# Performance work log

Hardware: AMD Instinct MI355X
Metric: run time of the kernel (lower is better)

## Reference

```python
import jax, jax.numpy as jnp
import numpy as np

B = 32768
D_VIS, D_LANG, D_STATE = 256, 128, 128
D_MODEL, N_EXP, TOP_K = 512, 8, 2
D_IN = D_VIS + D_LANG + D_STATE
EPS = 1e-5

def _gelu(x):
    # torch nn.GELU default = exact erf form
    return jax.nn.gelu(x, approximate=False)

def _ln(x, g, b):
    mu = x.mean(-1, keepdims=True)
    var = ((x - mu) ** 2).mean(-1, keepdims=True)
    return (x - mu) / jnp.sqrt(var + EPS) * g + b

def setup_inputs() -> dict:
    key = jax.random.key(0)
    ks = jax.random.split(key, 16)
    f32 = jnp.float32
    def w(k, shape, fan_in):
        return jax.random.normal(k, shape, dtype=f32) * (1.0 / np.sqrt(fan_in))
    return {
        "vis":   jax.random.normal(ks[0], (B, D_VIS), dtype=f32),
        "lang":  jax.random.normal(ks[1], (B, D_LANG), dtype=f32),
        "state": jax.random.normal(ks[2], (B, D_STATE), dtype=f32),
        # fusion: Linear(D_IN, D_MODEL) + LayerNorm + GELU
        "Wf": w(ks[3], (D_IN, D_MODEL), D_IN),
        "bf": jnp.zeros((D_MODEL,), f32),
        "gf": jnp.ones((D_MODEL,), f32),
        "betaf": jnp.zeros((D_MODEL,), f32),
        # gate (bias-free); random instead of torch's zeros-init so routing is non-degenerate
        "Wg": w(ks[4], (D_MODEL, N_EXP), D_MODEL),
        # stacked expert params: d -> 2d -> d -> d, residual LayerNorm
        "W1": w(ks[5], (N_EXP, D_MODEL, 2 * D_MODEL), D_MODEL),
        "b1": jnp.zeros((N_EXP, 2 * D_MODEL), f32),
        "W2": w(ks[6], (N_EXP, 2 * D_MODEL, D_MODEL), 2 * D_MODEL),
        "b2": jnp.zeros((N_EXP, D_MODEL), f32),
        "W3": w(ks[7], (N_EXP, D_MODEL, D_MODEL), D_MODEL),
        "b3": jnp.zeros((N_EXP, D_MODEL), f32),
        "ge": jnp.ones((N_EXP, D_MODEL), f32),
        "be": jnp.zeros((N_EXP, D_MODEL), f32),
    }

def reference(vis, lang, state, Wf, bf, gf, betaf, Wg, W1, b1, W2, b2, W3, b3, ge, be):
    # fusion projection  [B, D_IN] -> [B, D_MODEL]
    x = _gelu(_ln(jnp.concatenate([vis, lang, state], axis=-1) @ Wf + bf, gf, betaf))
    logits = x @ Wg                              # [B, E]
    all_probs = jax.nn.softmax(logits, axis=-1)  # [B, E]
    top_vals, top_idx = jax.lax.top_k(logits, TOP_K)   # [B, K]
    top_w = jax.nn.softmax(top_vals, axis=-1)          # [B, K]
    # per-(token, expert) combine weight: sum_k top_w[b,k] * [top_idx[b,k]==e]
    onehot = jax.nn.one_hot(top_idx, N_EXP, dtype=x.dtype)   # [B, K, E]
    combine = (onehot * top_w[..., None]).sum(axis=1)        # [B, E]
    out = jnp.zeros_like(x)
    for e in range(N_EXP):  # small fixed expert count; dense compute, sparse combine
        h = _gelu(x @ W1[e] + b1[e])
        h = _gelu(h @ W2[e] + b2[e])
        h = h @ W3[e] + b3[e]
        y = _ln(x + h, ge[e], be[e])            # Expert: ln(x + net(x))
        out = out + combine[:, e:e + 1] * y
    # load-balancing aux loss (counts carry no gradient, as in torch scatter_add of ones)
    counts = onehot.sum(axis=(0, 1))            # [E]
    f_i = counts / (B * TOP_K)
    lb_loss = N_EXP * jnp.sum(f_i * all_probs.mean(axis=0))
    return out, lb_loss
```

## Files before the change

kernel.cpp:

```cpp
#include <hip/hip_runtime.h>
#include <math.h>

typedef __bf16     bf16x8 __attribute__((ext_vector_type(8)));
typedef _Float16   f16x8  __attribute__((ext_vector_type(8)));
typedef float      f32x4  __attribute__((ext_vector_type(4)));
typedef unsigned short u16x8 __attribute__((ext_vector_type(8)));

#define DEVI __device__ __forceinline__
constexpr int B_TOK = 32768;
constexpr int MAXT  = 520;
constexpr int NBLK  = B_TOK / 16;

DEVI unsigned short f2bf(float f){
  unsigned int u = __builtin_bit_cast(unsigned int, f);
  u += 0x7fffu + ((u >> 16) & 1u);
  return (unsigned short)(u >> 16);
}
DEVI float bf2f(unsigned short b){
  return __builtin_bit_cast(float, (unsigned int)b << 16);
}
DEVI float gelu_fast(float x){
  float z = fabsf(x) * 0.70710678118654752f;
  float t = __builtin_amdgcn_rcpf(1.f + 0.3275911f * z);
  float p = t*(0.254829592f + t*(-0.284496736f + t*(1.421413741f + t*(-1.453152027f + t*1.061405429f))));
  float e = __expf(-z * z);
  float erfz = 1.f - p * e;
  float s = copysignf(erfz, x);
  return 0.5f * x * (1.f + s);
}
DEVI void load16_lds(const void* g, void* l){
  __builtin_amdgcn_global_load_lds(
      (const __attribute__((address_space(1))) unsigned int*)g,
      (__attribute__((address_space(3))) unsigned int*)l, 16, 0, 0);
}
DEVI float wredsum(float v){
#pragma unroll
  for (int off = 32; off > 0; off >>= 1) v += __shfl_xor(v, off, 64);
  return v;
}

__global__ void transpose_cast_bf16_k(const float* __restrict__ src, unsigned short* __restrict__ dst,
                                      int R, int C){
  __shared__ float tile[32][33];
  size_t base = (size_t)blockIdx.z * R * C;
  int c0 = blockIdx.x * 32, r0 = blockIdx.y * 32;
  for (int i = threadIdx.y; i < 32; i += 8)
    tile[i][threadIdx.x] = src[base + (size_t)(r0 + i) * C + c0 + threadIdx.x];
  __syncthreads();
  for (int i = threadIdx.y; i < 32; i += 8)
    dst[base + (size_t)(c0 + i) * R + r0 + threadIdx.x] = f2bf(tile[threadIdx.x][i]);
}

__global__ void transpose_split_f16_k(const float* __restrict__ src, unsigned short* __restrict__ dh,
                                      unsigned short* __restrict__ dl, int R, int C){
  __shared__ float tile[32][33];
  int c0 = blockIdx.x * 32, r0 = blockIdx.y * 32;
  for (int i = threadIdx.y; i < 32; i += 8)
    tile[i][threadIdx.x] = src[(size_t)(r0 + i) * C + c0 + threadIdx.x];
  __syncthreads();
  for (int i = threadIdx.y; i < 32; i += 8){
    float f = tile[threadIdx.x][i];
    _Float16 h = (_Float16)f;
    _Float16 l = (_Float16)(f - (float)h);
    size_t o = (size_t)(c0 + i) * R + r0 + threadIdx.x;
    dh[o] = __builtin_bit_cast(unsigned short, h);
    dl[o] = __builtin_bit_cast(unsigned short, l);
  }
}

__global__ __launch_bounds__(256, 2) void gemm_fusion_f16split(
    const float* __restrict__ vis, const float* __restrict__ lang, const float* __restrict__ state,
    const unsigned short* __restrict__ Wh, const unsigned short* __restrict__ Wl,
    const float* __restrict__ bias, float* __restrict__ Xpre)
{
  constexpr int K = 512, N = 512;
  __shared__ alignas(16) unsigned short smemF[32768];
  unsigned short* AhS = smemF;
  unsigned short* AlS = smemF + 8192;
  unsigned short* BhS = smemF + 16384;
  unsigned short* BlS = smemF + 24576;
  const int tid = threadIdx.x;
  const int row_s = tid >> 3, col_s = (tid & 7) * 8;
  const int swz = (row_s & 7) << 3;
  const unsigned short *pbh[4], *pbl[4];
  int arow[4];
#pragma unroll
  for (int i = 0; i < 4; ++i){
    arow[i] = blockIdx.x * 128 + i * 32 + row_s;
    size_t br = (size_t)(blockIdx.y * 128 + i * 32 + row_s) * K + (col_s ^ swz);
    pbh[i] = Wh + br; pbl[i] = Wl + br;
  }
  const int w = tid >> 6, lane = tid & 63;
  const int wr = (w >> 1) * 64, wc = (w & 1) * 64;
  const int lm = lane & 15, lk8 = (lane >> 4) * 8;
  const int fxor = (lm & 7) << 3;
  f32x4 acc[4][4] = {};
  for (int k0 = 0; k0 < K; k0 += 64){
#pragma unroll
    for (int i = 0; i < 4; ++i){
      load16_lds(pbh[i] + k0, &BhS[i*2048 + tid*8]);
      load16_lds(pbl[i] + k0, &BlS[i*2048 + tid*8]);
    }
    int col = k0 + col_s;
#pragma unroll
    for (int i = 0; i < 4; ++i){
      const float* src;
      if (col < 256)      src = vis   + (size_t)arow[i] * 256 + col;
      else if (col < 384) src = lang  + (size_t)arow[i] * 128 + (col - 256);
      else                src = state + (size_t)arow[i] * 128 + (col - 384);
      float4 a = *(const float4*)src, b = *(const float4*)(src + 4);
      float f[8] = {a.x, a.y, a.z, a.w, b.x, b.y, b.z, b.w};
      u16x8 hh, ll;
#pragma unroll
      for (int j = 0; j < 8; ++j){
        _Float16 h = (_Float16)f[j];
        _Float16 l = (_Float16)(f[j] - (float)h);
        hh[j] = __builtin_bit_cast(unsigned short, h);
        ll[j] = __builtin_bit_cast(unsigned short, l);
      }
      *(u16x8*)&AhS[i*2048 + row_s*64 + (col_s ^ swz)] = hh;
      *(u16x8*)&AlS[i*2048 + row_s*64 + (col_s ^ swz)] = ll;
    }
    __syncthreads();
#pragma unroll
    for (int kk = 0; kk < 64; kk += 32){
      f16x8 fah[4], fal[4], fbh[4], fbl[4];
#pragma unroll
      for (int m = 0; m < 4; ++m){
        int ro = (wr + m*16 + lm) * 64 + ((kk + lk8) ^ fxor);
        fah[m] = *(const f16x8*)&AhS[ro];
        fal[m] = *(const f16x8*)&AlS[ro];
      }
#pragma unroll
      for (int n = 0; n < 4; ++n){
        int ro = (wc + n*16 + lm) * 64 + ((kk + lk8) ^ fxor);
        fbh[n] = *(const f16x8*)&BhS[ro];
        fbl[n] = *(const f16x8*)&BlS[ro];
      }
#pragma unroll
      for (int m = 0; m < 4; ++m)
#pragma unroll
        for (int n = 0; n < 4; ++n){
          acc[m][n] = __builtin_amdgcn_mfma_f32_16x16x32_f16(fah[m], fbh[n], acc[m][n], 0, 0, 0);
          acc[m][n] = __builtin_amdgcn_mfma_f32_16x16x32_f16(fal[m], fbh[n], acc[m][n], 0, 0, 0);
          acc[m][n] = __builtin_amdgcn_mfma_f32_16x16x32_f16(fah[m], fbl[n], acc[m][n], 0, 0, 0);
        }
    }
    __syncthreads();
  }
  float* Cs = (float*)smemF;
  const int lk4 = (lane >> 4) * 4;
#pragma unroll
  for (int n = 0; n < 4; ++n){
    float bv = bias[blockIdx.y * 128 + wc + n*16 + lm];
#pragma unroll
    for (int m = 0; m < 4; ++m)
#pragma unroll
      for (int r = 0; r < 4; ++r){
        int rr = wr + m*16 + lk4 + r;
        Cs[rr * 128 + ((wc + n*16 + lm) ^ ((rr & 7) << 2))] = acc[m][n][r] + bv;
      }
  }
  __syncthreads();
#pragma unroll
  for (int j = 0; j < 16; ++j){
    int r = j*8 + (tid >> 5), c = (tid & 31) * 4;
    float4 v = *(const float4*)&Cs[r*128 + (c ^ ((r & 7) << 2))];
    *(float4*)&Xpre[(size_t)(blockIdx.x*128 + r) * N + blockIdx.y*128 + c] = v;
  }
}

template<int K, int N, int NT, bool GATHER, bool GELU_ACT, bool GLOBAL_ROW>
__global__ __launch_bounds__(256, 2) void egemm_k(
    const unsigned short* __restrict__ A, const int* __restrict__ rowlist,
    const int* __restrict__ cnt, const int* __restrict__ nTilesP,
    const int* __restrict__ tileE, const int* __restrict__ tileR0,
    int chunkBase, int chunkTiles, int tpg,
    const unsigned short* __restrict__ W, const float* __restrict__ bias,
    unsigned short* __restrict__ Cout)
{
  const int g = blockIdx.x & 7;
  const int j = blockIdx.x >> 3;
  const int tloc = g * tpg + j / NT;
  const int ntile = j % NT;
  if (tloc >= chunkTiles) return;
  const int t = chunkBase + tloc;
  if (t >= nTilesP[0]) return;
  const int e = tileE[t], r0 = tileR0[t];
  int rows = cnt[e] - r0; rows = rows > 128 ? 128 : rows;
  __shared__ alignas(16) unsigned short smem[16384];
  unsigned short* As = smem;
  unsigned short* Bs = smem + 8192;
  const int tid = threadIdx.x;
  const int row_s = tid >> 3, col_s = (tid & 7) * 8;
  const int swz = (row_s & 7) << 3;
  const unsigned short *pa[4], *pb[4];
#pragma unroll
  for (int i = 0; i < 4; ++i){
    int ir = i * 32 + row_s;
    size_t arow;
    if (GATHER){
      int rr = ir < rows ? ir : rows - 1;
      arow = (size_t)rowlist[(size_t)e * B_TOK + r0 + rr];
    } else {
      arow = (size_t)tloc * 128 + ir;
    }
    pa[i] = A + arow * K + (col_s ^ swz);
    pb[i] = W + (size_t)e * ((size_t)N * K) + (size_t)(ntile * 128 + ir) * K + (col_s ^ swz);
  }
  const int w = tid >> 6, lane = tid & 63;
  const int wr = (w >> 1) * 64, wc = (w & 1) * 64;
  const int lm = lane & 15, lk8 = (lane >> 4) * 8;
  const int fxor = (lm & 7) << 3;
  f32x4 acc[4][4] = {};
  for (int k0 = 0; k0 < K; k0 += 64){
#pragma unroll
    for (int i = 0; i < 4; ++i) load16_lds(pa[i] + k0, &As[i*2048 + tid*8]);
#pragma unroll
    for (int i = 0; i < 4; ++i) load16_lds(pb[i] + k0, &Bs[i*2048 + tid*8]);
    __syncthreads();
#pragma unroll
    for (int kk = 0; kk < 64; kk += 32){
      bf16x8 a[4], b[4];
#pragma unroll
      for (int m = 0; m < 4; ++m)
        a[m] = *(const bf16x8*)&As[(wr + m*16 + lm)*64 + ((kk + lk8) ^ fxor)];
#pragma unroll
      for (int n = 0; n < 4; ++n)
        b[n] = *(const bf16x8*)&Bs[(wc + n*16 + lm)*64 + ((kk + lk8) ^ fxor)];
#pragma unroll
      for (int m = 0; m < 4; ++m)
#pragma unroll
        for (int n = 0; n < 4; ++n)
          acc[m][n] = __builtin_amdgcn_mfma_f32_16x16x32_bf16(a[m], b[n], acc[m][n], 0, 0, 0);
    }
    __syncthreads();
  }
  unsigned short* Cs = smem;
  const int lk4 = (lane >> 4) * 4;
#pragma unroll
  for (int n = 0; n < 4; ++n){
    float bv = bias[(size_t)e * N + ntile * 128 + wc + n*16 + lm];
#pragma unroll
    for (int m = 0; m < 4; ++m)
#pragma unroll
      for (int r = 0; r < 4; ++r){
        float v = acc[m][n][r] + bv;
        if (GELU_ACT) v = gelu_fast(v);
        int rr = wr + m*16 + lk4 + r;
        Cs[rr * 128 + ((wc + n*16 + lm) ^ ((rr & 7) << 3))] = f2bf(v);
      }
  }
  __syncthreads();
  const size_t outTile = GLOBAL_ROW ? (size_t)t * 128 : (size_t)tloc * 128;
#pragma unroll
  for (int jj = 0; jj < 8; ++jj){
    int r = jj*16 + (tid >> 4), c = (tid & 15) * 8;
    if (r < rows){
      u16x8 v = *(const u16x8*)&Cs[r*128 + (c ^ ((r & 7) << 3))];
      *(u16x8*)&Cout[(outTile + r) * N + ntile*128 + c] = v;
    }
  }
}

__global__ __launch_bounds__(256) void ln_gelu_gate_k(
    const float* __restrict__ Xpre, const float* __restrict__ gf,
    const float* __restrict__ betaf, const float* __restrict__ Wg,
    unsigned short* __restrict__ Xbf, int* __restrict__ PK,
    int* __restrict__ BlockCnt, float* __restrict__ BlockProbs)
{
  __shared__ float s_probs[8];
  __shared__ int s_cnt[8];
  __shared__ int s_pk[16];
  __shared__ float s_w[16];
  const int tid = threadIdx.x, wv = tid >> 6, lane = tid & 63;
  if (tid < 8){ s_probs[tid] = 0.f; s_cnt[tid] = 0; }
  __syncthreads();
  float gg[8], bb[8], wg[8][8];
  {
    const float4* gp = (const float4*)(gf + lane * 8);
    const float4* bp = (const float4*)(betaf + lane * 8);
    float4 g0 = gp[0], g1 = gp[1], c0 = bp[0], c1 = bp[1];
    gg[0]=g0.x; gg[1]=g0.y; gg[2]=g0.z; gg[3]=g0.w; gg[4]=g1.x; gg[5]=g1.y; gg[6]=g1.z; gg[7]=g1.w;
    bb[0]=c0.x; bb[1]=c0.y; bb[2]=c0.z; bb[3]=c0.w; bb[4]=c1.x; bb[5]=c1.y; bb[6]=c1.z; bb[7]=c1.w;
#pragma unroll
    for (int j = 0; j < 8; ++j){
      const float4* wrow = (const float4*)(Wg + (size_t)(lane * 8 + j) * 8);
      float4 w0 = wrow[0], w1 = wrow[1];
      wg[j][0]=w0.x; wg[j][1]=w0.y; wg[j][2]=w0.z; wg[j][3]=w0.w;
      wg[j][4]=w1.x; wg[j][5]=w1.y; wg[j][6]=w1.z; wg[j][7]=w1.w;
    }
  }
  float4 vv[4][2];
#pragma unroll
  for (int it = 0; it < 4; ++it){
    const int row = blockIdx.x * 16 + wv * 4 + it;
    const float* xp = Xpre + (size_t)row * 512 + lane * 8;
    vv[it][0] = *(const float4*)xp;
    vv[it][1] = *(const float4*)(xp + 4);
  }
#pragma unroll
  for (int it = 0; it < 4; ++it){
    const int tloc = wv * 4 + it;
    const int row = blockIdx.x * 16 + tloc;
    float v[8] = {vv[it][0].x, vv[it][0].y, vv[it][0].z, vv[it][0].w,
                  vv[it][1].x, vv[it][1].y, vv[it][1].z, vv[it][1].w};
    float s1 = 0.f, s2 = 0.f;
#pragma unroll
    for (int j = 0; j < 8; ++j){ s1 += v[j]; s2 += v[j]*v[j]; }
    {
      float sel = (lane & 1) ? s1 : s2;
      float r = __shfl_xor(sel, 1, 64);
      float tt = ((lane & 1) ? s2 : s1) + r;
#pragma unroll
      for (int off = 2; off < 64; off <<= 1) tt += __shfl_xor(tt, off, 64);
      float other = __shfl_xor(tt, 1, 64);
      s1 = (lane & 1) ? other : tt;
      s2 = (lane & 1) ? tt : other;
    }
    const float mu  = s1 * (1.f / 512.f);
    const float var = s2 * (1.f / 512.f) - mu * mu;
    const float inv = 1.f / sqrtf(var + 1e-5f);
    float o[8];
#pragma unroll
    for (int j = 0; j < 8; ++j)
      o[j] = gelu_fast((v[j] - mu) * inv * gg[j] + bb[j]);
    u16x8 ob;
#pragma unroll
    for (int j = 0; j < 8; ++j) ob[j] = f2bf(o[j]);
    *(u16x8*)(Xbf + (size_t)row * 512 + lane * 8) = ob;
    float acc[8] = {0.f,0.f,0.f,0.f,0.f,0.f,0.f,0.f};
#pragma unroll
    for (int j = 0; j < 8; ++j)
#pragma unroll
      for (int e = 0; e < 8; ++e) acc[e] += o[j] * wg[j][e];
    float v4[4], v2[2], v1f;
#pragma unroll
    for (int i = 0; i < 4; ++i){
      float sel = (lane & 1) ? acc[i] : acc[i+4];
      float r = __shfl_xor(sel, 1, 64);
      v4[i] = ((lane & 1) ? acc[i+4] : acc[i]) + r;
    }
#pragma unroll
    for (int i = 0; i < 2; ++i){
      float sel = (lane & 2) ? v4[i] : v4[i+2];
      float r = __shfl_xor(sel, 2, 64);
      v2[i] = ((lane & 2) ? v4[i+2] : v4[i]) + r;
    }
    {
      float sel = (lane & 4) ? v2[0] : v2[1];
      float r = __shfl_xor(sel, 4, 64);
      v1f = ((lane & 4) ? v2[1] : v2[0]) + r;
    }
#pragma unroll
    for (int off = 8; off < 64; off <<= 1) v1f += __shfl_xor(v1f, off, 64);
    float lg[8];
#pragma unroll
    for (int e = 0; e < 8; ++e){
      int src = (lane & 56) | ((e >> 2) & 1) | (((e >> 1) & 1) << 1) | ((e & 1) << 2);
      lg[e] = __shfl(v1f, src, 64);
    }
    float mx = lg[0];
#pragma unroll
    for (int e = 1; e < 8; ++e) mx = fmaxf(mx, lg[e]);
    float pe[8], ps = 0.f;
#pragma unroll
    for (int e = 0; e < 8; ++e){ pe[e] = __expf(lg[e] - mx); ps += pe[e]; }
    float invp = 1.f / ps;
    int i1 = 0;
#pragma unroll
    for (int e = 1; e < 8; ++e) if (lg[e] > lg[i1]) i1 = e;
    int i2 = (i1 == 0) ? 1 : 0;
#pragma unroll
    for (int e = 0; e < 8; ++e) if (e != i1 && lg[e] > lg[i2]) i2 = e;
    float wA = 1.f / (1.f + __expf(lg[i2] - lg[i1]));
    if (lane == 0){
#pragma unroll
      for (int e = 0; e < 8; ++e) atomicAdd(&s_probs[e], pe[e] * invp);
      int r0 = atomicAdd(&s_cnt[i1], 1);
      int r1 = atomicAdd(&s_cnt[i2], 1);
      s_pk[tloc] = i1 | (r0 << 3) | (i2 << 8) | (r1 << 16);
      s_w[tloc] = wA;
    }
  }
  __syncthreads();
  if (tid < 8){
    BlockCnt[blockIdx.x * 8 + tid] = s_cnt[tid];
    BlockProbs[blockIdx.x * 8 + tid] = s_probs[tid];
  }
  if (tid < 16){
    int t = blockIdx.x * 16 + tid;
    PK[2*t]   = s_pk[tid];
    PK[2*t+1] = __builtin_bit_cast(int, s_w[tid]);
  }
}

__global__ __launch_bounds__(256) void scan_k(
    const int* __restrict__ BlockCnt, const float* __restrict__ BlockProbs,
    int* __restrict__ BlockBase, int* __restrict__ CNT, int* __restrict__ nTiles,
    int* __restrict__ tileE, int* __restrict__ tileR0, int* __restrict__ rowBase,
    float* __restrict__ lbOut)
{
  __shared__ int sS[8][256];
  __shared__ float sF[8][256];
  __shared__ int sTot[8];
  __shared__ float sProbTot[8];
  __shared__ int sTileBase[9];
  const int tid = threadIdx.x;
  int local[8][8];
  int sum[8] = {0,0,0,0,0,0,0,0};
  float fsum[8] = {0.f,0.f,0.f,0.f,0.f,0.f,0.f,0.f};
#pragma unroll
  for (int jb = 0; jb < 8; ++jb){
    int blk = tid * 8 + jb;
#pragma unroll
    for (int e = 0; e < 8; ++e){
      int c = BlockCnt[blk*8 + e];
      local[jb][e] = c;
      sum[e] += c;
      fsum[e] += BlockProbs[blk*8 + e];
    }
  }
#pragma unroll
  for (int e = 0; e < 8; ++e){ sS[e][tid] = sum[e]; sF[e][tid] = fsum[e]; }
  __syncthreads();
  for (int off = 1; off < 256; off <<= 1){
    int add[8];
#pragma unroll
    for (int e = 0; e < 8; ++e) add[e] = (tid >= off) ? sS[e][tid - off] : 0;
    __syncthreads();
#pragma unroll
    for (int e = 0; e < 8; ++e) sS[e][tid] += add[e];
    __syncthreads();
  }
  for (int off = 128; off > 0; off >>= 1){
    if (tid < off)
#pragma unroll
      for (int e = 0; e < 8; ++e) sF[e][tid] += sF[e][tid + off];
    __syncthreads();
  }
  int base[8];
#pragma unroll
  for (int e = 0; e < 8; ++e) base[e] = (tid == 0) ? 0 : sS[e][tid-1];
#pragma unroll
  for (int jb = 0; jb < 8; ++jb){
    int blk = tid * 8 + jb;
#pragma unroll
    for (int e = 0; e < 8; ++e){ BlockBase[blk*8 + e] = base[e]; base[e] += local[jb][e]; }
  }
  if (tid == 0){
    int t = 0;
    float acc = 0.f;
    for (int e = 0; e < 8; ++e){
      int c = sS[e][255]; c = c < 0 ? 0 : (c > B_TOK ? B_TOK : c);
      sTot[e] = c;
      CNT[e] = c;
      sTileBase[e] = t;
      rowBase[e] = t * 128;
      t += (c + 127) >> 7;
      acc += ((float)c / (float)(B_TOK * 2)) * (sF[e][0] / (float)B_TOK);
    }
    sTileBase[8] = t;
    nTiles[0] = t;
    lbOut[0] = 8.f * acc;
  }
  __syncthreads();
  const int ntot = sTileBase[8];
  for (int i = tid; i < MAXT; i += 256){
    int e = 0;
#pragma unroll
    for (int k = 1; k <= 8; ++k) if (i >= sTileBase[k]) e = k;
    if (i < ntot){ tileE[i] = e; tileR0[i] = (i - sTileBase[e]) * 128; }
    else { tileE[i] = 0; tileR0[i] = 0; }
  }
}

__global__ __launch_bounds__(256) void place_k(
    const int* __restrict__ PK, const int* __restrict__ BlockBase,
    int* __restrict__ rowlist, int* __restrict__ TS, float* __restrict__ TW)
{
  const int t = blockIdx.x * 256 + threadIdx.x;
  int pk = PK[2*t];
  float w0 = __builtin_bit_cast(float, PK[2*t+1]);
  int e0 = pk & 7, r0 = (pk >> 3) & 31;
  int e1 = (pk >> 8) & 7, r1 = (pk >> 16) & 31;
  int blk = t >> 4;
  int p0 = BlockBase[blk*8 + e0] + r0;
  int p1 = BlockBase[blk*8 + e1] + r1;
  rowlist[(size_t)e0 * B_TOK + p0] = t;
  rowlist[(size_t)e1 * B_TOK + p1] = t;
  TS[2*t]   = (e0 << 15) | p0;  TW[2*t]   = w0;
  TS[2*t+1] = (e1 << 15) | p1;  TW[2*t+1] = 1.f - w0;
}

__global__ __launch_bounds__(256) void combine_k(
    const unsigned short* __restrict__ Xbf, const unsigned short* __restrict__ H3F,
    const int* __restrict__ TS, const float* __restrict__ TW,
    const int* __restrict__ rowBase, const float* __restrict__ ge,
    const float* __restrict__ be, float* __restrict__ out)
{
  const int tok = blockIdx.x * 4 + (threadIdx.x >> 6);
  const int lane = threadIdx.x & 63;
  u16x8 xb = *(const u16x8*)(Xbf + (size_t)tok * 512 + lane * 8);
  float x[8];
#pragma unroll
  for (int j = 0; j < 8; ++j) x[j] = bf2f(xb[j]);
  float o[8] = {0.f,0.f,0.f,0.f,0.f,0.f,0.f,0.f};
#pragma unroll
  for (int kslot = 0; kslot < 2; ++kslot){
    int sl = TS[tok*2 + kslot];
    float wgt = TW[tok*2 + kslot];
    int e = sl >> 15, p = sl & 32767;
    size_t hrow = (size_t)(rowBase[e] + p);
    u16x8 hb = *(const u16x8*)(H3F + hrow * 512 + lane * 8);
    float s[8];
#pragma unroll
    for (int j = 0; j < 8; ++j) s[j] = x[j] + bf2f(hb[j]);
    float sm = 0.f;
#pragma unroll
    for (int j = 0; j < 8; ++j) sm += s[j];
    sm = wredsum(sm);
    float mu = sm * (1.f / 512.f);
    float q = 0.f;
#pragma unroll
    for (int j = 0; j < 8; ++j){ float d = s[j] - mu; q += d * d; }
    q = wredsum(q);
    float inv = 1.f / sqrtf(q * (1.f / 512.f) + 1e-5f);
    const float4* gp = (const float4*)(ge + (size_t)e * 512 + lane * 8);
    const float4* bp = (const float4*)(be + (size_t)e * 512 + lane * 8);
    float4 g0 = gp[0], g1 = gp[1], c0 = bp[0], c1 = bp[1];
    float gg[8] = {g0.x,g0.y,g0.z,g0.w,g1.x,g1.y,g1.z,g1.w};
    float bb[8] = {c0.x,c0.y,c0.z,c0.w,c1.x,c1.y,c1.z,c1.w};
#pragma unroll
    for (int j = 0; j < 8; ++j)
      o[j] += wgt * ((s[j]-mu)*inv*gg[j] + bb[j]);
  }
  float* op = out + (size_t)tok * 512 + lane * 8;
  *(float4*)op       = make_float4(o[0], o[1], o[2], o[3]);
  *(float4*)(op + 4) = make_float4(o[4], o[5], o[6], o[7]);
}

extern "C" void kernel_launch(void* const* d_in, const int* in_sizes, int n_in,
                              void* d_out, int out_size, void* d_ws, size_t ws_size,
                              hipStream_t stream)
{
  (void)in_sizes; (void)n_in; (void)out_size;
  const float* vis   = (const float*)d_in[0];
  const float* lang  = (const float*)d_in[1];
  const float* state = (const float*)d_in[2];
  const float* Wf    = (const float*)d_in[3];
  const float* bf    = (const float*)d_in[4];
  const float* gf    = (const float*)d_in[5];
  const float* betaf = (const float*)d_in[6];
  const float* Wg    = (const float*)d_in[7];
  const float* W1    = (const float*)d_in[8];
  const float* b1    = (const float*)d_in[9];
  const float* W2    = (const float*)d_in[10];
  const float* b2    = (const float*)d_in[11];
  const float* W3    = (const float*)d_in[12];
  const float* b3    = (const float*)d_in[13];
  const float* ge    = (const float*)d_in[14];
  const float* be    = (const float*)d_in[15];

  char* ws = (char*)d_ws;
  size_t off = 0;
  auto alloc = [&](size_t n){ size_t o = off; off += (n + 255) & ~(size_t)255; return o; };

  unsigned short* WFH  = (unsigned short*)(ws + alloc((size_t)512*512*2));
  unsigned short* WFL  = (unsigned short*)(ws + alloc((size_t)512*512*2));
  unsigned short* W1T  = (unsigned short*)(ws + alloc((size_t)8*1024*512*2));
  unsigned short* W2T  = (unsigned short*)(ws + alloc((size_t)8*512*1024*2));
  unsigned short* W3T  = (unsigned short*)(ws + alloc((size_t)8*512*512*2));
  unsigned short* XBF  = (unsigned short*)(ws + alloc((size_t)B_TOK*512*2));
  int*            RLIST= (int*)(ws + alloc((size_t)8*B_TOK*4));
  int*            TS   = (int*)(ws + alloc((size_t)B_TOK*2*4));
  float*          TW   = (float*)(ws + alloc((size_t)B_TOK*2*4));
  int*            PK   = (int*)(ws + alloc((size_t)B_TOK*2*4));
  int*            BCNT = (int*)(ws + alloc((size_t)NBLK*8*4));
  float*          BPROB= (float*)(ws + alloc((size_t)NBLK*8*4));
  int*            BBASE= (int*)(ws + alloc((size_t)NBLK*8*4));
  int*            CNT  = (int*)(ws + alloc(64));
  int*            NT_  = (int*)(ws + alloc(64));
  int*            RB   = (int*)(ws + alloc(64));
  int*            TE   = (int*)(ws + alloc(MAXT*4));
  int*            TR   = (int*)(ws + alloc(MAXT*4));
  unsigned short* H3F  = (unsigned short*)(ws + alloc((size_t)MAXT*128*512*2));

  const size_t perTile = (size_t)128*1024*2 + (size_t)128*512*2;
  size_t remain = (ws_size > off) ? (ws_size - off) : 0;
  int tch, nch;
  size_t need2 = (size_t)260 * perTile, need4 = (size_t)B_TOK*512*4;
  if (remain >= need2 && need2 >= need4){ tch = 260; nch = 2; }
  else { tch = 130; nch = 4; }
  size_t regB = alloc(need2 > need4 ? (nch == 2 ? need2 : need4) : need4);
  float*          XPRE = (float*)(ws + regB);
  unsigned short* H1   = (unsigned short*)(ws + regB);
  unsigned short* H2   = H1 + (size_t)tch*128*1024;
  const int tpg = (tch + 7) / 8;

  transpose_split_f16_k<<<dim3(16,16,1), dim3(32,8), 0, stream>>>(Wf, WFH, WFL, 512, 512);
  transpose_cast_bf16_k<<<dim3(32,16,8), dim3(32,8), 0, stream>>>(W1, W1T, 512, 1024);
  transpose_cast_bf16_k<<<dim3(16,32,8), dim3(32,8), 0, stream>>>(W2, W2T, 1024, 512);
  transpose_cast_bf16_k<<<dim3(16,16,8), dim3(32,8), 0, stream>>>(W3, W3T, 512, 512);
  gemm_fusion_f16split<<<dim3(256,4), 256, 0, stream>>>(vis, lang, state, WFH, WFL, bf, XPRE);
  ln_gelu_gate_k<<<NBLK, 256, 0, stream>>>(XPRE, gf, betaf, Wg, XBF, PK, BCNT, BPROB);
  scan_k<<<1, 256, 0, stream>>>(BCNT, BPROB, BBASE, CNT, NT_, TE, TR, RB,
                                ((float*)d_out) + (size_t)B_TOK*512);
  place_k<<<B_TOK/256, 256, 0, stream>>>(PK, BBASE, RLIST, TS, TW);

  for (int c = 0; c < nch; ++c){
    int cb = c * tch;
    egemm_k<512, 1024, 8, true,  true,  false><<<dim3(8*tpg*8), 256, 0, stream>>>(
        XBF, RLIST, CNT, NT_, TE, TR, cb, tch, tpg, W1T, b1, H1);
    egemm_k<1024, 512, 4, false, true,  false><<<dim3(8*tpg*4), 256, 0, stream>>>(
        H1,  RLIST, CNT, NT_, TE, TR, cb, tch, tpg, W2T, b2, H2);
    egemm_k<512,  512, 4, false, false, true ><<<dim3(8*tpg*4), 256, 0, stream>>>(
        H2,  RLIST, CNT, NT_, TE, TR, cb, tch, tpg, W3T, b3, H3F);
  }
  combine_k<<<B_TOK/4, 256, 0, stream>>>(XBF, H3F, TS, TW, RB, ge, be, (float*)d_out);
}
```

Baseline: 470.5 us.

## Fuse fusion GEMM with LayerNorm, GELU and gating into one kernel

The fusion projection GEMM now computes full 512-wide rows per 128-token block with 512 threads. LayerNorm, GELU, gate logits, softmax and top-2 selection run in the epilogue from registers. This removes the fp32 Xpre round trip through global memory and a separate kernel launch. Routing blocks grow from 16 to 128 tokens, so the scan and place kernels and the PK bit packing are adapted. The cost is about 97KB of LDS per block and a heavier register load, which lowers occupancy, and the grid shrinks to 256 blocks.

```diff
diff --git a/kernel.cpp b/kernel.cpp
--- a/kernel.cpp
+++ b/kernel.cpp
@@ -9,7 +9,7 @@
 #define DEVI __device__ __forceinline__
 constexpr int B_TOK = 32768;
 constexpr int MAXT  = 520;
-constexpr int NBLK  = B_TOK / 16;
+constexpr int NBLK  = B_TOK / 128;
 
 DEVI unsigned short f2bf(float f){
   unsigned int u = __builtin_bit_cast(unsigned int, f);
@@ -68,48 +68,60 @@
   }
 }
 
-__global__ __launch_bounds__(256, 2) void gemm_fusion_f16split(
+__global__ __launch_bounds__(512, 2) void fusion_mega_k(
     const float* __restrict__ vis, const float* __restrict__ lang, const float* __restrict__ state,
     const unsigned short* __restrict__ Wh, const unsigned short* __restrict__ Wl,
-    const float* __restrict__ bias, float* __restrict__ Xpre)
+    const float* __restrict__ bias, const float* __restrict__ gf, const float* __restrict__ betaf,
+    const float* __restrict__ Wg, unsigned short* __restrict__ Xbf, int* __restrict__ PK,
+    int* __restrict__ BlockCnt, float* __restrict__ BlockProbs)
 {
-  constexpr int K = 512, N = 512;
-  __shared__ alignas(16) unsigned short smemF[32768];
-  unsigned short* AhS = smemF;
-  unsigned short* AlS = smemF + 8192;
-  unsigned short* BhS = smemF + 16384;
-  unsigned short* BlS = smemF + 24576;
+  __shared__ alignas(16) unsigned char LDS[98816];
+  unsigned short* AhS = (unsigned short*)LDS;
+  unsigned short* AlS = (unsigned short*)(LDS + 8192);
+  unsigned short* BhS = (unsigned short*)(LDS + 16384);
+  unsigned short* BlS = (unsigned short*)(LDS + 49152);
+  float*          part= (float*)(LDS + 81920);
+  float*          lgP = (float*)(LDS + 81920);
+  unsigned short* xT  = (unsigned short*)LDS;
+  __shared__ float s_probs[8];
+  __shared__ int   s_cnt[8];
+  __shared__ int   s_pk[128];
+  __shared__ float s_w[128];
+
   const int tid = threadIdx.x;
-  const int row_s = tid >> 3, col_s = (tid & 7) * 8;
-  const int swz = (row_s & 7) << 3;
-  const unsigned short *pbh[4], *pbl[4];
-  int arow[4];
-#pragma unroll
-  for (int i = 0; i < 4; ++i){
-    arow[i] = blockIdx.x * 128 + i * 32 + row_s;
-    size_t br = (size_t)(blockIdx.y * 128 + i * 32 + row_s) * K + (col_s ^ swz);
-    pbh[i] = Wh + br; pbl[i] = Wl + br;
-  }
-  const int w = tid >> 6, lane = tid & 63;
-  const int wr = (w >> 1) * 64, wc = (w & 1) * 64;
-  const int lm = lane & 15, lk8 = (lane >> 4) * 8;
-  const int fxor = (lm & 7) << 3;
-  f32x4 acc[4][4] = {};
-  for (int k0 = 0; k0 < K; k0 += 64){
-#pragma unroll
-    for (int i = 0; i < 4; ++i){
-      load16_lds(pbh[i] + k0, &BhS[i*2048 + tid*8]);
-      load16_lds(pbl[i] + k0, &BlS[i*2048 + tid*8]);
-    }
-    int col = k0 + col_s;
-#pragma unroll
-    for (int i = 0; i < 4; ++i){
+  const int lane = tid & 63;
+  const int w = tid >> 6;
+  const int rowg = w >> 2, colw = w & 3;
+  const int lm = lane & 15;
+  const int oct = lane >> 4;
+  const int lk4 = oct * 4;
+  if (tid < 8){ s_cnt[tid] = 0; s_probs[tid] = 0.f; }
+
+  const int arow_l = tid >> 2;
+  const size_t arow_g = (size_t)blockIdx.x * 128 + arow_l;
+  const int acol8 = (tid & 3) * 8;
+  const int adst  = arow_l * 32 + ((((acol8 >> 3) ^ (arow_l & 3))) << 3);
+  const int brow0 = tid >> 2;
+  const int bswz  = (((tid & 3) ^ ((tid >> 2) & 3)) << 3);
+
+  f32x4 acc[4][8] = {};
+  for (int k0 = 0; k0 < 512; k0 += 32){
+#pragma unroll
+    for (int rd = 0; rd < 4; ++rd){
+      int row = rd * 128 + brow0;
+      size_t so = (size_t)row * 512 + k0 + bswz;
+      int d8 = (rd * 512 + tid) * 8;
+      load16_lds(Wh + so, &BhS[d8]);
+      load16_lds(Wl + so, &BlS[d8]);
+    }
+    {
+      int k = k0 + acol8;
       const float* src;
-      if (col < 256)      src = vis   + (size_t)arow[i] * 256 + col;
-      else if (col < 384) src = lang  + (size_t)arow[i] * 128 + (col - 256);
-      else                src = state + (size_t)arow[i] * 128 + (col - 384);
-      float4 a = *(const float4*)src, b = *(const float4*)(src + 4);
-      float f[8] = {a.x, a.y, a.z, a.w, b.x, b.y, b.z, b.w};
+      if (k < 256)      src = vis   + arow_g * 256 + k;
+      else if (k < 384) src = lang  + arow_g * 128 + (k - 256);
+      else              src = state + arow_g * 128 + (k - 384);
+      float4 a0 = *(const float4*)src, a1 = *(const float4*)(src + 4);
+      float f[8] = {a0.x, a0.y, a0.z, a0.w, a1.x, a1.y, a1.z, a1.w};
       u16x8 hh, ll;
 #pragma unroll
       for (int j = 0; j < 8; ++j){
@@ -118,55 +130,195 @@
         hh[j] = __builtin_bit_cast(unsigned short, h);
         ll[j] = __builtin_bit_cast(unsigned short, l);
       }
-      *(u16x8*)&AhS[i*2048 + row_s*64 + (col_s ^ swz)] = hh;
-      *(u16x8*)&AlS[i*2048 + row_s*64 + (col_s ^ swz)] = ll;
-    }
-    __syncthreads();
-#pragma unroll
-    for (int kk = 0; kk < 64; kk += 32){
-      f16x8 fah[4], fal[4], fbh[4], fbl[4];
-#pragma unroll
-      for (int m = 0; m < 4; ++m){
-        int ro = (wr + m*16 + lm) * 64 + ((kk + lk8) ^ fxor);
-        fah[m] = *(const f16x8*)&AhS[ro];
-        fal[m] = *(const f16x8*)&AlS[ro];
+      *(u16x8*)&AhS[adst] = hh;
+      *(u16x8*)&AlS[adst] = ll;
+    }
+    __syncthreads();
+    f16x8 fah[4], fal[4];
+#pragma unroll
+    for (int m = 0; m < 4; ++m){
+      int row = rowg * 64 + m * 16 + lm;
+      int ro = row * 32 + ((oct ^ (lm & 3)) << 3);
+      fah[m] = *(const f16x8*)&AhS[ro];
+      fal[m] = *(const f16x8*)&AlS[ro];
+    }
+#pragma unroll
+    for (int nh = 0; nh < 2; ++nh){
+      f16x8 fbh[4], fbl[4];
+#pragma unroll
+      for (int nn = 0; nn < 4; ++nn){
+        int nrow = colw * 128 + (nh * 4 + nn) * 16 + lm;
+        int ro = nrow * 32 + ((oct ^ (lm & 3)) << 3);
+        fbh[nn] = *(const f16x8*)&BhS[ro];
+        fbl[nn] = *(const f16x8*)&BlS[ro];
       }
 #pragma unroll
-      for (int n = 0; n < 4; ++n){
-        int ro = (wc + n*16 + lm) * 64 + ((kk + lk8) ^ fxor);
-        fbh[n] = *(const f16x8*)&BhS[ro];
-        fbl[n] = *(const f16x8*)&BlS[ro];
+      for (int m = 0; m < 4; ++m)
+#pragma unroll
+        for (int nn = 0; nn < 4; ++nn){
+          int n = nh * 4 + nn;
+          acc[m][n] = __builtin_amdgcn_mfma_f32_16x16x32_f16(fah[m], fbh[nn], acc[m][n], 0, 0, 0);
+          acc[m][n] = __builtin_amdgcn_mfma_f32_16x16x32_f16(fal[m], fbh[nn], acc[m][n], 0, 0, 0);
+          acc[m][n] = __builtin_amdgcn_mfma_f32_16x16x32_f16(fah[m], fbl[nn], acc[m][n], 0, 0, 0);
+        }
+    }
+    __syncthreads();
+  }
+
+  float bvn[8], gn[8], btn[8];
+#pragma unroll
+  for (int n = 0; n < 8; ++n){
+    int c = colw * 128 + n * 16 + lm;
+    bvn[n] = bias[c]; gn[n] = gf[c]; btn[n] = betaf[c];
+  }
+  float s1v[16], s2v[16];
+#pragma unroll
+  for (int m = 0; m < 4; ++m)
+#pragma unroll
+    for (int r = 0; r < 4; ++r){
+      float s1 = 0.f, s2 = 0.f;
+#pragma unroll
+      for (int n = 0; n < 8; ++n){
+        float v = acc[m][n][r] + bvn[n];
+        s1 += v; s2 += v * v;
       }
+      s1v[m*4+r] = s1; s2v[m*4+r] = s2;
+    }
+#pragma unroll
+  for (int off = 1; off < 16; off <<= 1)
+#pragma unroll
+    for (int i = 0; i < 16; ++i){
+      s1v[i] += __shfl_xor(s1v[i], off, 64);
+      s2v[i] += __shfl_xor(s2v[i], off, 64);
+    }
+  if (lm == 0){
+#pragma unroll
+    for (int m = 0; m < 4; ++m)
+#pragma unroll
+      for (int r = 0; r < 4; ++r){
+        int row = rowg * 64 + m * 16 + lk4 + r;
+        part[(row * 4 + colw) * 2]     = s1v[m*4+r];
+        part[(row * 4 + colw) * 2 + 1] = s2v[m*4+r];
+      }
+  }
+  __syncthreads();
+  float muv[16], invv[16];
+#pragma unroll
+  for (int m = 0; m < 4; ++m)
+#pragma unroll
+    for (int r = 0; r < 4; ++r){
+      int row = rowg * 64 + m * 16 + lk4 + r;
+      float s1 = part[row*8] + part[row*8+2] + part[row*8+4] + part[row*8+6];
+      float s2 = part[row*8+1] + part[row*8+3] + part[row*8+5] + part[row*8+7];
+      float mu = s1 * (1.f/512.f);
+      float var = s2 * (1.f/512.f) - mu * mu;
+      muv[m*4+r] = mu;
+      invv[m*4+r] = 1.f / sqrtf(var + 1e-5f);
+    }
+  __syncthreads();
+#pragma unroll
+  for (int m = 0; m < 4; ++m)
+#pragma unroll
+    for (int n = 0; n < 8; ++n)
+#pragma unroll
+      for (int r = 0; r < 4; ++r)
+        acc[m][n][r] = gelu_fast((acc[m][n][r] + bvn[n] - muv[m*4+r]) * invv[m*4+r] * gn[n] + btn[n]);
+  float wgv[8][8];
+#pragma unroll
+  for (int n = 0; n < 8; ++n){
+    int c = colw * 128 + n * 16 + lm;
+    float4 w0 = *(const float4*)&Wg[(size_t)c * 8];
+    float4 w1 = *(const float4*)&Wg[(size_t)c * 8 + 4];
+    wgv[n][0]=w0.x; wgv[n][1]=w0.y; wgv[n][2]=w0.z; wgv[n][3]=w0.w;
+    wgv[n][4]=w1.x; wgv[n][5]=w1.y; wgv[n][6]=w1.z; wgv[n][7]=w1.w;
+  }
+#pragma unroll
+  for (int e = 0; e < 8; ++e){
+    float p[16];
+#pragma unroll
+    for (int m = 0; m < 4; ++m)
+#pragma unroll
+      for (int r = 0; r < 4; ++r){
+        float s = 0.f;
+#pragma unroll
+        for (int n = 0; n < 8; ++n) s += acc[m][n][r] * wgv[n][e];
+        p[m*4+r] = s;
+      }
+#pragma unroll
+    for (int off = 1; off < 16; off <<= 1)
+#pragma unroll
+      for (int i = 0; i < 16; ++i) p[i] += __shfl_xor(p[i], off, 64);
+    if (lm == 0){
 #pragma unroll
       for (int m = 0; m < 4; ++m)
 #pragma unroll
-        for (int n = 0; n < 4; ++n){
-          acc[m][n] = __builtin_amdgcn_mfma_f32_16x16x32_f16(fah[m], fbh[n], acc[m][n], 0, 0, 0);
-          acc[m][n] = __builtin_amdgcn_mfma_f32_16x16x32_f16(fal[m], fbh[n], acc[m][n], 0, 0, 0);
-          acc[m][n] = __builtin_amdgcn_mfma_f32_16x16x32_f16(fah[m], fbl[n], acc[m][n], 0, 0, 0);
+        for (int r = 0; r < 4; ++r){
+          int row = rowg * 64 + m * 16 + lk4 + r;
+          lgP[row * 33 + colw * 8 + e] = p[m*4+r];
         }
     }
-    __syncthreads();
-  }
-  float* Cs = (float*)smemF;
-  const int lk4 = (lane >> 4) * 4;
-#pragma unroll
-  for (int n = 0; n < 4; ++n){
-    float bv = bias[blockIdx.y * 128 + wc + n*16 + lm];
-#pragma unroll
-    for (int m = 0; m < 4; ++m)
-#pragma unroll
-      for (int r = 0; r < 4; ++r){
-        int rr = wr + m*16 + lk4 + r;
-        Cs[rr * 128 + ((wc + n*16 + lm) ^ ((rr & 7) << 2))] = acc[m][n][r] + bv;
-      }
-  }
-  __syncthreads();
-#pragma unroll
-  for (int j = 0; j < 16; ++j){
-    int r = j*8 + (tid >> 5), c = (tid & 31) * 4;
-    float4 v = *(const float4*)&Cs[r*128 + (c ^ ((r & 7) << 2))];
-    *(float4*)&Xpre[(size_t)(blockIdx.x*128 + r) * N + blockIdx.y*128 + c] = v;
+  }
+  __syncthreads();
+#pragma unroll
+  for (int pp = 0; pp < 2; ++pp){
+    if (rowg == pp){
+#pragma unroll
+      for (int m = 0; m < 4; ++m)
+#pragma unroll
+        for (int n = 0; n < 8; ++n)
+#pragma unroll
+          for (int r = 0; r < 4; ++r){
+            int lr = m * 16 + lk4 + r;
+            int col = colw * 128 + n * 16 + lm;
+            xT[lr * 512 + (col ^ ((lr & 7) << 3))] = f2bf(acc[m][n][r]);
+          }
+    }
+    __syncthreads();
+#pragma unroll
+    for (int rr = 0; rr < 8; ++rr){
+      int idx = rr * 512 + tid;
+      int row = idx >> 6, c8 = (idx & 63) * 8;
+      u16x8 v = *(const u16x8*)&xT[row * 512 + (c8 ^ ((row & 7) << 3))];
+      *(u16x8*)&Xbf[((size_t)blockIdx.x * 128 + pp * 64 + row) * 512 + c8] = v;
+    }
+    __syncthreads();
+  }
+  if (tid < 128){
+    const int tk = tid;
+    float lg[8];
+#pragma unroll
+    for (int e = 0; e < 8; ++e)
+      lg[e] = lgP[tk*33 + e] + lgP[tk*33 + 8 + e] + lgP[tk*33 + 16 + e] + lgP[tk*33 + 24 + e];
+    float mx = lg[0];
+#pragma unroll
+    for (int e = 1; e < 8; ++e) mx = fmaxf(mx, lg[e]);
+    float pe[8], ps = 0.f;
+#pragma unroll
+    for (int e = 0; e < 8; ++e){ pe[e] = __expf(lg[e] - mx); ps += pe[e]; }
+    float invp = 1.f / ps;
+#pragma unroll
+    for (int e = 0; e < 8; ++e) atomicAdd(&s_probs[e], pe[e] * invp);
+    int i1 = 0;
+#pragma unroll
+    for (int e = 1; e < 8; ++e) if (lg[e] > lg[i1]) i1 = e;
+    int i2 = (i1 == 0) ? 1 : 0;
+#pragma unroll
+    for (int e = 0; e < 8; ++e) if (e != i1 && lg[e] > lg[i2]) i2 = e;
+    float wA = 1.f / (1.f + __expf(lg[i2] - lg[i1]));
+    int r0 = atomicAdd(&s_cnt[i1], 1);
+    int r1 = atomicAdd(&s_cnt[i2], 1);
+    s_pk[tk] = i1 | (r0 << 3) | (i2 << 10) | (r1 << 13);
+    s_w[tk]  = wA;
+  }
+  __syncthreads();
+  if (tid < 8){
+    BlockCnt[blockIdx.x * 8 + tid] = s_cnt[tid];
+    BlockProbs[blockIdx.x * 8 + tid] = s_probs[tid];
+  }
+  if (tid < 128){
+    int t = blockIdx.x * 128 + tid;
+    PK[2*t]   = s_pk[tid];
+    PK[2*t+1] = __builtin_bit_cast(int, s_w[tid]);
   }
 }
 
@@ -263,138 +415,6 @@
   }
 }
 
-__global__ __launch_bounds__(256) void ln_gelu_gate_k(
-    const float* __restrict__ Xpre, const float* __restrict__ gf,
-    const float* __restrict__ betaf, const float* __restrict__ Wg,
-    unsigned short* __restrict__ Xbf, int* __restrict__ PK,
-    int* __restrict__ BlockCnt, float* __restrict__ BlockProbs)
-{
-  __shared__ float s_probs[8];
-  __shared__ int s_cnt[8];
-  __shared__ int s_pk[16];
-  __shared__ float s_w[16];
-  const int tid = threadIdx.x, wv = tid >> 6, lane = tid & 63;
-  if (tid < 8){ s_probs[tid] = 0.f; s_cnt[tid] = 0; }
-  __syncthreads();
-  float gg[8], bb[8], wg[8][8];
-  {
-    const float4* gp = (const float4*)(gf + lane * 8);
-    const float4* bp = (const float4*)(betaf + lane * 8);
-    float4 g0 = gp[0], g1 = gp[1], c0 = bp[0], c1 = bp[1];
-    gg[0]=g0.x; gg[1]=g0.y; gg[2]=g0.z; gg[3]=g0.w; gg[4]=g1.x; gg[5]=g1.y; gg[6]=g1.z; gg[7]=g1.w;
-    bb[0]=c0.x; bb[1]=c0.y; bb[2]=c0.z; bb[3]=c0.w; bb[4]=c1.x; bb[5]=c1.y; bb[6]=c1.z; bb[7]=c1.w;
-#pragma unroll
-    for (int j = 0; j < 8; ++j){
-      const float4* wrow = (const float4*)(Wg + (size_t)(lane * 8 + j) * 8);
-      float4 w0 = wrow[0], w1 = wrow[1];
-      wg[j][0]=w0.x; wg[j][1]=w0.y; wg[j][2]=w0.z; wg[j][3]=w0.w;
-      wg[j][4]=w1.x; wg[j][5]=w1.y; wg[j][6]=w1.z; wg[j][7]=w1.w;
-    }
-  }
-  float4 vv[4][2];
-#pragma unroll
-  for (int it = 0; it < 4; ++it){
-    const int row = blockIdx.x * 16 + wv * 4 + it;
-    const float* xp = Xpre + (size_t)row * 512 + lane * 8;
-    vv[it][0] = *(const float4*)xp;
-    vv[it][1] = *(const float4*)(xp + 4);
-  }
-#pragma unroll
-  for (int it = 0; it < 4; ++it){
-    const int tloc = wv * 4 + it;
-    const int row = blockIdx.x * 16 + tloc;
-    float v[8] = {vv[it][0].x, vv[it][0].y, vv[it][0].z, vv[it][0].w,
-                  vv[it][1].x, vv[it][1].y, vv[it][1].z, vv[it][1].w};
-    float s1 = 0.f, s2 = 0.f;
-#pragma unroll
-    for (int j = 0; j < 8; ++j){ s1 += v[j]; s2 += v[j]*v[j]; }
-    {
-      float sel = (lane & 1) ? s1 : s2;
-      float r = __shfl_xor(sel, 1, 64);
-      float tt = ((lane & 1) ? s2 : s1) + r;
-#pragma unroll
-      for (int off = 2; off < 64; off <<= 1) tt += __shfl_xor(tt, off, 64);
-      float other = __shfl_xor(tt, 1, 64);
-      s1 = (lane & 1) ? other : tt;
-      s2 = (lane & 1) ? tt : other;
-    }
-    const float mu  = s1 * (1.f / 512.f);
-    const float var = s2 * (1.f / 512.f) - mu * mu;
-    const float inv = 1.f / sqrtf(var + 1e-5f);
-    float o[8];
-#pragma unroll
-    for (int j = 0; j < 8; ++j)
-      o[j] = gelu_fast((v[j] - mu) * inv * gg[j] + bb[j]);
-    u16x8 ob;
-#pragma unroll
-    for (int j = 0; j < 8; ++j) ob[j] = f2bf(o[j]);
-    *(u16x8*)(Xbf + (size_t)row * 512 + lane * 8) = ob;
-    float acc[8] = {0.f,0.f,0.f,0.f,0.f,0.f,0.f,0.f};
-#pragma unroll
-    for (int j = 0; j < 8; ++j)
-#pragma unroll
-      for (int e = 0; e < 8; ++e) acc[e] += o[j] * wg[j][e];
-    float v4[4], v2[2], v1f;
-#pragma unroll
-    for (int i = 0; i < 4; ++i){
-      float sel = (lane & 1) ? acc[i] : acc[i+4];
-      float r = __shfl_xor(sel, 1, 64);
-      v4[i] = ((lane & 1) ? acc[i+4] : acc[i]) + r;
-    }
-#pragma unroll
-    for (int i = 0; i < 2; ++i){
-      float sel = (lane & 2) ? v4[i] : v4[i+2];
-      float r = __shfl_xor(sel, 2, 64);
-      v2[i] = ((lane & 2) ? v4[i+2] : v4[i]) + r;
-    }
-    {
-      float sel = (lane & 4) ? v2[0] : v2[1];
-      float r = __shfl_xor(sel, 4, 64);
-      v1f = ((lane & 4) ? v2[1] : v2[0]) + r;
-    }
-#pragma unroll
-    for (int off = 8; off < 64; off <<= 1) v1f += __shfl_xor(v1f, off, 64);
-    float lg[8];
-#pragma unroll
-    for (int e = 0; e < 8; ++e){
-      int src = (lane & 56) | ((e >> 2) & 1) | (((e >> 1) & 1) << 1) | ((e & 1) << 2);
-      lg[e] = __shfl(v1f, src, 64);
-    }
-    float mx = lg[0];
-#pragma unroll
-    for (int e = 1; e < 8; ++e) mx = fmaxf(mx, lg[e]);
-    float pe[8], ps = 0.f;
-#pragma unroll
-    for (int e = 0; e < 8; ++e){ pe[e] = __expf(lg[e] - mx); ps += pe[e]; }
-    float invp = 1.f / ps;
-    int i1 = 0;
-#pragma unroll
-    for (int e = 1; e < 8; ++e) if (lg[e] > lg[i1]) i1 = e;
-    int i2 = (i1 == 0) ? 1 : 0;
-#pragma unroll
-    for (int e = 0; e < 8; ++e) if (e != i1 && lg[e] > lg[i2]) i2 = e;
-    float wA = 1.f / (1.f + __expf(lg[i2] - lg[i1]));
-    if (lane == 0){
-#pragma unroll
-      for (int e = 0; e < 8; ++e) atomicAdd(&s_probs[e], pe[e] * invp);
-      int r0 = atomicAdd(&s_cnt[i1], 1);
-      int r1 = atomicAdd(&s_cnt[i2], 1);
-      s_pk[tloc] = i1 | (r0 << 3) | (i2 << 8) | (r1 << 16);
-      s_w[tloc] = wA;
-    }
-  }
-  __syncthreads();
-  if (tid < 8){
-    BlockCnt[blockIdx.x * 8 + tid] = s_cnt[tid];
-    BlockProbs[blockIdx.x * 8 + tid] = s_probs[tid];
-  }
-  if (tid < 16){
-    int t = blockIdx.x * 16 + tid;
-    PK[2*t]   = s_pk[tid];
-    PK[2*t+1] = __builtin_bit_cast(int, s_w[tid]);
-  }
-}
-
 __global__ __launch_bounds__(256) void scan_k(
     const int* __restrict__ BlockCnt, const float* __restrict__ BlockProbs,
     int* __restrict__ BlockBase, int* __restrict__ CNT, int* __restrict__ nTiles,
@@ -403,26 +423,15 @@
 {
   __shared__ int sS[8][256];
   __shared__ float sF[8][256];
-  __shared__ int sTot[8];
-  __shared__ float sProbTot[8];
   __shared__ int sTileBase[9];
   const int tid = threadIdx.x;
-  int local[8][8];
-  int sum[8] = {0,0,0,0,0,0,0,0};
-  float fsum[8] = {0.f,0.f,0.f,0.f,0.f,0.f,0.f,0.f};
-#pragma unroll
-  for (int jb = 0; jb < 8; ++jb){
-    int blk = tid * 8 + jb;
-#pragma unroll
-    for (int e = 0; e < 8; ++e){
-      int c = BlockCnt[blk*8 + e];
-      local[jb][e] = c;
-      sum[e] += c;
-      fsum[e] += BlockProbs[blk*8 + e];
-    }
-  }
-#pragma unroll
-  for (int e = 0; e < 8; ++e){ sS[e][tid] = sum[e]; sF[e][tid] = fsum[e]; }
+  int loc[8];
+#pragma unroll
+  for (int e = 0; e < 8; ++e){
+    loc[e] = BlockCnt[tid*8 + e];
+    sS[e][tid] = loc[e];
+    sF[e][tid] = BlockProbs[tid*8 + e];
+  }
   __syncthreads();
   for (int off = 1; off < 256; off <<= 1){
     int add[8];
@@ -439,21 +448,14 @@
       for (int e = 0; e < 8; ++e) sF[e][tid] += sF[e][tid + off];
     __syncthreads();
   }
-  int base[8];
-#pragma unroll
-  for (int e = 0; e < 8; ++e) base[e] = (tid == 0) ? 0 : sS[e][tid-1];
-#pragma unroll
-  for (int jb = 0; jb < 8; ++jb){
-    int blk = tid * 8 + jb;
-#pragma unroll
-    for (int e = 0; e < 8; ++e){ BlockBase[blk*8 + e] = base[e]; base[e] += local[jb][e]; }
-  }
+#pragma unroll
+  for (int e = 0; e < 8; ++e)
+    BlockBase[tid*8 + e] = sS[e][tid] - loc[e];
   if (tid == 0){
     int t = 0;
     float acc = 0.f;
     for (int e = 0; e < 8; ++e){
       int c = sS[e][255]; c = c < 0 ? 0 : (c > B_TOK ? B_TOK : c);
-      sTot[e] = c;
       CNT[e] = c;
       sTileBase[e] = t;
       rowBase[e] = t * 128;
@@ -482,9 +484,9 @@
   const int t = blockIdx.x * 256 + threadIdx.x;
   int pk = PK[2*t];
   float w0 = __builtin_bit_cast(float, PK[2*t+1]);
-  int e0 = pk & 7, r0 = (pk >> 3) & 31;
-  int e1 = (pk >> 8) & 7, r1 = (pk >> 16) & 31;
-  int blk = t >> 4;
+  int e0 = pk & 7, r0 = (pk >> 3) & 127;
+  int e1 = (pk >> 10) & 7, r1 = (pk >> 13) & 127;
+  int blk = t >> 7;
   int p0 = BlockBase[blk*8 + e0] + r0;
   int p1 = BlockBase[blk*8 + e1] + r1;
   rowlist[(size_t)e0 * B_TOK + p0] = t;
@@ -588,12 +590,9 @@
 
   const size_t perTile = (size_t)128*1024*2 + (size_t)128*512*2;
   size_t remain = (ws_size > off) ? (ws_size - off) : 0;
-  int tch, nch;
-  size_t need2 = (size_t)260 * perTile, need4 = (size_t)B_TOK*512*4;
-  if (remain >= need2 && need2 >= need4){ tch = 260; nch = 2; }
-  else { tch = 130; nch = 4; }
-  size_t regB = alloc(need2 > need4 ? (nch == 2 ? need2 : need4) : need4);
-  float*          XPRE = (float*)(ws + regB);
+  const int tch = (remain >= (size_t)260 * perTile) ? 260 : 130;
+  const int nch = (tch == 260) ? 2 : 4;
+  size_t regB = alloc((size_t)tch * perTile);
   unsigned short* H1   = (unsigned short*)(ws + regB);
   unsigned short* H2   = H1 + (size_t)tch*128*1024;
   const int tpg = (tch + 7) / 8;
@@ -602,8 +601,8 @@
   transpose_cast_bf16_k<<<dim3(32,16,8), dim3(32,8), 0, stream>>>(W1, W1T, 512, 1024);
   transpose_cast_bf16_k<<<dim3(16,32,8), dim3(32,8), 0, stream>>>(W2, W2T, 1024, 512);
   transpose_cast_bf16_k<<<dim3(16,16,8), dim3(32,8), 0, stream>>>(W3, W3T, 512, 512);
-  gemm_fusion_f16split<<<dim3(256,4), 256, 0, stream>>>(vis, lang, state, WFH, WFL, bf, XPRE);
-  ln_gelu_gate_k<<<NBLK, 256, 0, stream>>>(XPRE, gf, betaf, Wg, XBF, PK, BCNT, BPROB);
+  fusion_mega_k<<<NBLK, 512, 0, stream>>>(vis, lang, state, WFH, WFL, bf, gf, betaf, Wg,
+                                          XBF, PK, BCNT, BPROB);
   scan_k<<<1, 256, 0, stream>>>(BCNT, BPROB, BBASE, CNT, NT_, TE, TR, RB,
                                 ((float*)d_out) + (size_t)B_TOK*512);
   place_k<<<B_TOK/256, 256, 0, stream>>>(PK, BBASE, RLIST, TS, TW);
```

Result: slower. 611.9 us (+30.1%).
